# Kernel tuning notes

Hardware: AMD Instinct MI355X
Metric: run time of the kernel (lower is better)

The kernel has to match this reference:

```python
import jax, jax.numpy as jnp
import numpy as np

N_NODES = 170000
N_EDGES = 1200000
IN_C, HID_C, OUT_C = 128, 128, 40
BN_EPS = 1e-5


def setup_inputs() -> dict:
    key = jax.random.key(0)
    ks = jax.random.split(key, 12)
    def glorot(k, fan_in, fan_out):
        lim = (6.0 / (fan_in + fan_out)) ** 0.5
        return jax.random.uniform(k, (fan_in, fan_out), jnp.float32, -lim, lim)
    x = jax.random.normal(ks[0], (N_NODES, IN_C), jnp.float32)
    edge_index = jax.random.randint(ks[1], (2, N_EDGES), 0, N_NODES, jnp.int64)
    return {
        "x": x,
        "edge_index": edge_index,
        "W0": glorot(ks[2], IN_C, HID_C), "b0": jnp.zeros((HID_C,), jnp.float32),
        "g0": jnp.ones((HID_C,), jnp.float32), "be0": jnp.zeros((HID_C,), jnp.float32),
        "W1": glorot(ks[3], HID_C, HID_C), "b1": jnp.zeros((HID_C,), jnp.float32),
        "g1": jnp.ones((HID_C,), jnp.float32), "be1": jnp.zeros((HID_C,), jnp.float32),
        "W2": glorot(ks[4], HID_C, OUT_C), "b2": jnp.zeros((OUT_C,), jnp.float32),
    }


def _gcn_norm(edge_index, num_nodes):
    # add self-loops, symmetric normalization (PyG GCNConv default)
    loop = jnp.arange(num_nodes, dtype=edge_index.dtype)
    src = jnp.concatenate([edge_index[0], loop])
    dst = jnp.concatenate([edge_index[1], loop])
    deg = jax.ops.segment_sum(jnp.ones_like(dst, jnp.float32), dst, num_segments=num_nodes)
    dinv = jnp.where(deg > 0, jax.lax.rsqrt(deg), 0.0)
    norm = dinv[src] * dinv[dst]  # [E+N]
    return src, dst, norm


def _conv(h, W, b, src, dst, norm, num_nodes):
    h = h @ W                              # [N, out]
    msg = h[src] * norm[:, None]           # gather + scale, [E+N, out]
    out = jax.ops.segment_sum(msg, dst, num_segments=num_nodes)
    return out + b


def _bn_relu(h, g, be):
    mean = jnp.mean(h, axis=0)
    var = jnp.mean(jnp.square(h - mean), axis=0)  # biased, as torch BN training
    h = (h - mean) * jax.lax.rsqrt(var + BN_EPS) * g + be
    return jax.nn.relu(h)


def reference(x, edge_index, W0, b0, g0, be0, W1, b1, g1, be1, W2, b2):
    N = x.shape[0]
    src, dst, norm = _gcn_norm(edge_index, N)
    h = _bn_relu(_conv(x, W0, b0, src, dst, norm, N), g0, be0)
    h = _bn_relu(_conv(h, W1, b1, src, dst, norm, N), g1, be1)
    return _conv(h, W2, b2, src, dst, norm, N)
```

## Files before the change

### kernel.cpp

```cpp
#include <hip/hip_runtime.h>

#define BN_EPS 1e-5f
#define CAP 3072

using bf16x8 = __attribute__((ext_vector_type(8))) short;
using f32x4  = __attribute__((ext_vector_type(4))) float;

__device__ __forceinline__ unsigned int f2bf(float f) {
    unsigned int u = __float_as_uint(f);
    u += 0x7fffu + ((u >> 16) & 1u);
    return u >> 16;
}
__device__ __forceinline__ float bflo(unsigned int u) { return __uint_as_float(u << 16); }
__device__ __forceinline__ float bfhi(unsigned int u) { return __uint_as_float(u & 0xffff0000u); }

__global__ __launch_bounds__(1024) void k_init(int* __restrict__ bcur,
                                               float* __restrict__ stats, int NB) {
    int t = threadIdx.x;
    if (t < NB) bcur[t] = t * CAP;
    if (t < 512) stats[t] = 0.f;
}

__global__ __launch_bounds__(256) void k_bscatter(const int* __restrict__ ei,
                                                  int* __restrict__ bcur,
                                                  unsigned int* __restrict__ ebuf,
                                                  int E, int NB) {
    __shared__ int h[768];
    __shared__ int wb[768];
    for (int i = threadIdx.x; i < 768; i += 256) h[i] = 0;
    __syncthreads();
    int base = blockIdx.x * 8192;
    int rk[32];
    #pragma unroll
    for (int it = 0; it < 32; ++it) {
        int e = base + it * 256 + threadIdx.x;
        rk[it] = (e < E) ? atomicAdd(&h[ei[E + e] >> 8], 1) : 0;
    }
    __syncthreads();
    for (int i = threadIdx.x; i < NB; i += 256) {
        int c = h[i];
        wb[i] = c ? atomicAdd(&bcur[i], c) : 0;
    }
    __syncthreads();
    #pragma unroll
    for (int it = 0; it < 32; ++it) {
        int e = base + it * 256 + threadIdx.x;
        if (e < E) {
            unsigned s = (unsigned)ei[e], d = (unsigned)ei[E + e];
            int bk = (int)(d >> 8);
            int pos = wb[bk] + rk[it];
            if (pos < (bk + 1) * CAP)
                ebuf[pos] = s | ((d & 255u) << 24);
        }
    }
}

__global__ __launch_bounds__(256) void k_bfinal(const unsigned int* __restrict__ ebuf,
                                                const int* __restrict__ bcur,
                                                int* __restrict__ csr,
                                                int* __restrict__ rs,
                                                int* __restrict__ re,
                                                float* __restrict__ dinv, int N) {
    __shared__ int cnt[256];
    __shared__ int scn[256];
    __shared__ int cur[256];
    const int t = threadIdx.x, b = blockIdx.x;
    const int beg = b * CAP;
    const int cntE = min(bcur[b] - beg, CAP);
    cnt[t] = 0;
    __syncthreads();
    for (int j = t; j < cntE; j += 256)
        atomicAdd(&cnt[ebuf[beg + j] >> 24], 1);
    __syncthreads();
    int v = cnt[t];
    scn[t] = v;
    __syncthreads();
    for (int off = 1; off < 256; off <<= 1) {
        int x = (t >= off) ? scn[t - off] : 0;
        __syncthreads();
        scn[t] += x;
        __syncthreads();
    }
    int excl = scn[t] - v;
    int node = b * 256 + t;
    if (node < N) {
        rs[node]   = beg + excl;
        re[node]   = beg + excl + v;
        dinv[node] = rsqrtf((float)(1 + v));
    }
    cur[t] = beg + excl;
    __syncthreads();
    for (int j = t; j < cntE; j += 256) {
        unsigned e = ebuf[beg + j];
        int pos = atomicAdd(&cur[e >> 24], 1);
        csr[pos] = (int)(e & 0x00FFFFFFu);
    }
}

__global__ __launch_bounds__(256) void k_prepW3(const float* __restrict__ W0,
                                                const float* __restrict__ W1,
                                                const float* __restrict__ W2,
                                                unsigned short* __restrict__ Wf) {
    int t = blockIdx.x * 256 + threadIdx.x;
    int wid = t >> 11;
    int f = t & 2047;
    const float* W = (wid == 0) ? W0 : (wid == 1) ? W1 : W2;
    int C = (wid == 2) ? 40 : 128;
    int lane = f & 63, frag = f >> 6;
    int kt = frag & 3, ct = frag >> 2;
    int r = lane & 15, q = lane >> 4;
    int col = ct * 16 + r;
    int kbase = kt * 32 + q * 8;
    unsigned int v[8];
    #pragma unroll
    for (int j = 0; j < 8; ++j)
        v[j] = (col < C) ? f2bf(W[(size_t)(kbase + j) * C + col]) : 0u;
    uint4 o;
    o.x = v[0] | (v[1] << 16);
    o.y = v[2] | (v[3] << 16);
    o.z = v[4] | (v[5] << 16);
    o.w = v[6] | (v[7] << 16);
    ((uint4*)Wf)[t] = o;
}

__device__ __forceinline__ float bn_apply(float v, int c, const float* stats,
                                          const float* g, const float* be, float invN) {
    float mean = stats[c] * invN;
    float var  = fmaf(-mean, mean, stats[128 + c] * invN);
    float sc   = g[c] * rsqrtf(var + BN_EPS);
    float r    = fmaf(v - mean, sc, be[c]);
    return fmaxf(r, 0.0f);
}

template <int NOCT, int OST>
__global__ __launch_bounds__(256) void k_gemm_mfma(
        const void* __restrict__ X, int xf32, const unsigned short* __restrict__ Wf,
        unsigned short* __restrict__ H, int N,
        const float* __restrict__ stats, const float* __restrict__ g,
        const float* __restrict__ be) {
    __shared__ unsigned short aF[16 * 512];
    __shared__ unsigned short bF[NOCT * 4 * 512];
    const int tid = threadIdx.x;
    const int rowbase = blockIdx.x * 64;
    const float invN = 1.0f / (float)N;

    {
        const uint4* src = (const uint4*)Wf;
        uint4* dst = (uint4*)bF;
        #pragma unroll
        for (int i = 0; i < NOCT; ++i) dst[tid + 256 * i] = src[tid + 256 * i];
    }
    #pragma unroll
    for (int it = 0; it < 4; ++it) {
        int f = tid + 256 * it;
        int lane = f & 63, frag = f >> 6;
        int kt = frag & 3, rt = frag >> 2;
        int r = lane & 15, q = lane >> 4;
        int row = rowbase + rt * 16 + r;
        int kc = kt * 32 + q * 8;
        float vv[8];
        if (row < N) {
            if (xf32) {
                const float4* xp = (const float4*)((const float*)X + (size_t)row * 128 + kc);
                float4 p0 = xp[0], p1 = xp[1];
                vv[0] = p0.x; vv[1] = p0.y; vv[2] = p0.z; vv[3] = p0.w;
                vv[4] = p1.x; vv[5] = p1.y; vv[6] = p1.z; vv[7] = p1.w;
            } else {
                uint4 p = *((const uint4*)((const unsigned short*)X + (size_t)row * 128 + kc));
                vv[0] = bflo(p.x); vv[1] = bfhi(p.x);
                vv[2] = bflo(p.y); vv[3] = bfhi(p.y);
                vv[4] = bflo(p.z); vv[5] = bfhi(p.z);
                vv[6] = bflo(p.w); vv[7] = bfhi(p.w);
            }
            if (stats) {
                #pragma unroll
                for (int j = 0; j < 8; ++j)
                    vv[j] = bn_apply(vv[j], kc + j, stats, g, be, invN);
            }
        } else {
            #pragma unroll
            for (int j = 0; j < 8; ++j) vv[j] = 0.0f;
        }
        uint4 o;
        o.x = f2bf(vv[0]) | (f2bf(vv[1]) << 16);
        o.y = f2bf(vv[2]) | (f2bf(vv[3]) << 16);
        o.z = f2bf(vv[4]) | (f2bf(vv[5]) << 16);
        o.w = f2bf(vv[6]) | (f2bf(vv[7]) << 16);
        ((uint4*)aF)[f] = o;
    }
    __syncthreads();

    const int wave = tid >> 6, lane = tid & 63;
    f32x4 acc[NOCT];
    #pragma unroll
    for (int ct = 0; ct < NOCT; ++ct) acc[ct] = (f32x4){0.f, 0.f, 0.f, 0.f};

    #pragma unroll
    for (int kt = 0; kt < 4; ++kt) {
        bf16x8 a = ((const bf16x8*)aF)[(wave * 4 + kt) * 64 + lane];
        #pragma unroll
        for (int ct = 0; ct < NOCT; ++ct) {
            bf16x8 b = ((const bf16x8*)bF)[(ct * 4 + kt) * 64 + lane];
            acc[ct] = __builtin_amdgcn_mfma_f32_16x16x32_bf16(a, b, acc[ct], 0, 0, 0);
        }
    }

    const int q = lane >> 4, r = lane & 15;
    #pragma unroll
    for (int ct = 0; ct < NOCT; ++ct) {
        #pragma unroll
        for (int i = 0; i < 4; ++i) {
            int row = rowbase + wave * 16 + q * 4 + i;
            if (row < N)
                H[(size_t)row * OST + ct * 16 + r] = (unsigned short)f2bf(acc[ct][i]);
        }
    }
}

__global__ __launch_bounds__(256) void k_agg128(
        const unsigned short* __restrict__ H, const int* __restrict__ rs,
        const int* __restrict__ re, const int* __restrict__ csr,
        const float* __restrict__ dinv, const float* __restrict__ b,
        unsigned short* __restrict__ outb, int N) {
    int lane = threadIdx.x & 15;
    int node = blockIdx.x * 16 + (threadIdx.x >> 4);
    if (node >= N) return;
    float dd  = dinv[node];
    int   beg = rs[node];
    int   end = re[node];
    uint4 hp  = ((const uint4*)(H + (size_t)node * 128))[lane];
    float4 bb0 = ((const float4*)b)[lane * 2];
    float4 bb1 = ((const float4*)b)[lane * 2 + 1];
    float sl = dd * dd;
    float a0 = fmaf(bflo(hp.x), sl, bb0.x), a1 = fmaf(bfhi(hp.x), sl, bb0.y);
    float a2 = fmaf(bflo(hp.y), sl, bb0.z), a3 = fmaf(bfhi(hp.y), sl, bb0.w);
    float a4 = fmaf(bflo(hp.z), sl, bb1.x), a5 = fmaf(bfhi(hp.z), sl, bb1.y);
    float a6 = fmaf(bflo(hp.w), sl, bb1.z), a7 = fmaf(bfhi(hp.w), sl, bb1.w);
    int j = beg;
    for (; j + 2 <= end; j += 2) {
        int s0 = csr[j], s1 = csr[j + 1];
        float n0 = dinv[s0] * dd, n1 = dinv[s1] * dd;
        uint4 v0 = ((const uint4*)(H + (size_t)s0 * 128))[lane];
        uint4 v1 = ((const uint4*)(H + (size_t)s1 * 128))[lane];
        a0 = fmaf(bflo(v0.x), n0, fmaf(bflo(v1.x), n1, a0));
        a1 = fmaf(bfhi(v0.x), n0, fmaf(bfhi(v1.x), n1, a1));
        a2 = fmaf(bflo(v0.y), n0, fmaf(bflo(v1.y), n1, a2));
        a3 = fmaf(bfhi(v0.y), n0, fmaf(bfhi(v1.y), n1, a3));
        a4 = fmaf(bflo(v0.z), n0, fmaf(bflo(v1.z), n1, a4));
        a5 = fmaf(bfhi(v0.z), n0, fmaf(bfhi(v1.z), n1, a5));
        a6 = fmaf(bflo(v0.w), n0, fmaf(bflo(v1.w), n1, a6));
        a7 = fmaf(bfhi(v0.w), n0, fmaf(bfhi(v1.w), n1, a7));
    }
    if (j < end) {
        int s0 = csr[j];
        float n0 = dinv[s0] * dd;
        uint4 v0 = ((const uint4*)(H + (size_t)s0 * 128))[lane];
        a0 = fmaf(bflo(v0.x), n0, a0); a1 = fmaf(bfhi(v0.x), n0, a1);
        a2 = fmaf(bflo(v0.y), n0, a2); a3 = fmaf(bfhi(v0.y), n0, a3);
        a4 = fmaf(bflo(v0.z), n0, a4); a5 = fmaf(bfhi(v0.z), n0, a5);
        a6 = fmaf(bflo(v0.w), n0, a6); a7 = fmaf(bfhi(v0.w), n0, a7);
    }
    uint4 o;
    o.x = f2bf(a0) | (f2bf(a1) << 16);
    o.y = f2bf(a2) | (f2bf(a3) << 16);
    o.z = f2bf(a4) | (f2bf(a5) << 16);
    o.w = f2bf(a6) | (f2bf(a7) << 16);
    ((uint4*)(outb + (size_t)node * 128))[lane] = o;
}

__global__ __launch_bounds__(256) void k_agg40(
        const unsigned short* __restrict__ H, const int* __restrict__ rs,
        const int* __restrict__ re, const int* __restrict__ csr,
        const float* __restrict__ dinv, const float* __restrict__ b,
        float* __restrict__ out, int N) {
    int lane = threadIdx.x & 15;
    int node = blockIdx.x * 16 + (threadIdx.x >> 4);
    if (node >= N || lane >= 10) return;
    float dd  = dinv[node];
    int   beg = rs[node];
    int   end = re[node];
    uint2 hp  = ((const uint2*)(H + (size_t)node * 48))[lane];
    float4 bb = ((const float4*)b)[lane];
    float  sl = dd * dd;
    float4 acc = make_float4(fmaf(bflo(hp.x), sl, bb.x), fmaf(bfhi(hp.x), sl, bb.y),
                             fmaf(bflo(hp.y), sl, bb.z), fmaf(bfhi(hp.y), sl, bb.w));
    int j = beg;
    for (; j + 2 <= end; j += 2) {
        int s0 = csr[j], s1 = csr[j + 1];
        float n0 = dinv[s0] * dd, n1 = dinv[s1] * dd;
        uint2 v0 = ((const uint2*)(H + (size_t)s0 * 48))[lane];
        uint2 v1 = ((const uint2*)(H + (size_t)s1 * 48))[lane];
        acc.x = fmaf(bflo(v0.x), n0, fmaf(bflo(v1.x), n1, acc.x));
        acc.y = fmaf(bfhi(v0.x), n0, fmaf(bfhi(v1.x), n1, acc.y));
        acc.z = fmaf(bflo(v0.y), n0, fmaf(bflo(v1.y), n1, acc.z));
        acc.w = fmaf(bfhi(v0.y), n0, fmaf(bfhi(v1.y), n1, acc.w));
    }
    if (j < end) {
        int s0 = csr[j];
        float n0 = dinv[s0] * dd;
        uint2 v0 = ((const uint2*)(H + (size_t)s0 * 48))[lane];
        acc.x = fmaf(bflo(v0.x), n0, acc.x);
        acc.y = fmaf(bfhi(v0.x), n0, acc.y);
        acc.z = fmaf(bflo(v0.y), n0, acc.z);
        acc.w = fmaf(bfhi(v0.y), n0, acc.w);
    }
    ((float4*)(out + (size_t)node * 40))[lane] = acc;
}

__global__ __launch_bounds__(256) void k_bnstats(
        const unsigned short* __restrict__ Bb, float* __restrict__ stats, int N) {
    __shared__ float red[2][16][128];
    const int t = threadIdx.x;
    const int lane16 = t & 15, grp = t >> 4;
    const int cbase = lane16 * 8;
    float s[8], q[8];
    #pragma unroll
    for (int k = 0; k < 8; ++k) { s[k] = 0.f; q[k] = 0.f; }

    const int step = gridDim.x * 16;
    for (int r = blockIdx.x * 16 + grp; r < N; r += 2 * step) {
        uint4 p0 = *((const uint4*)(Bb + (size_t)r * 128 + cbase));
        int r1 = r + step;
        if (r1 < N) {
            uint4 p1 = *((const uint4*)(Bb + (size_t)r1 * 128 + cbase));
            float v[8] = {bflo(p1.x), bfhi(p1.x), bflo(p1.y), bfhi(p1.y),
                          bflo(p1.z), bfhi(p1.z), bflo(p1.w), bfhi(p1.w)};
            #pragma unroll
            for (int k = 0; k < 8; ++k) { s[k] += v[k]; q[k] = fmaf(v[k], v[k], q[k]); }
        }
        float u[8] = {bflo(p0.x), bfhi(p0.x), bflo(p0.y), bfhi(p0.y),
                      bflo(p0.z), bfhi(p0.z), bflo(p0.w), bfhi(p0.w)};
        #pragma unroll
        for (int k = 0; k < 8; ++k) { s[k] += u[k]; q[k] = fmaf(u[k], u[k], q[k]); }
    }
    #pragma unroll
    for (int k = 0; k < 8; ++k) {
        red[0][grp][cbase + k] = s[k];
        red[1][grp][cbase + k] = q[k];
    }
    __syncthreads();
    if (t < 128) {
        float acc = 0.f;
        #pragma unroll
        for (int g = 0; g < 16; ++g) acc += red[0][g][t];
        unsafeAtomicAdd(&stats[t], acc);
    } else {
        int c = t - 128;
        float acc = 0.f;
        #pragma unroll
        for (int g = 0; g < 16; ++g) acc += red[1][g][c];
        unsafeAtomicAdd(&stats[128 + c], acc);
    }
}

extern "C" void kernel_launch(void* const* d_in, const int* in_sizes, int n_in,
                              void* d_out, int out_size, void* d_ws, size_t ws_size,
                              hipStream_t stream) {
    const float* x   = (const float*)d_in[0];
    const int*   ei  = (const int*)d_in[1];
    const float* W0  = (const float*)d_in[2];
    const float* b0  = (const float*)d_in[3];
    const float* g0  = (const float*)d_in[4];
    const float* be0 = (const float*)d_in[5];
    const float* W1  = (const float*)d_in[6];
    const float* b1  = (const float*)d_in[7];
    const float* g1  = (const float*)d_in[8];
    const float* be1 = (const float*)d_in[9];
    const float* W2  = (const float*)d_in[10];
    const float* b2  = (const float*)d_in[11];
    float* out = (float*)d_out;

    const int N  = in_sizes[0] / 128;
    const int E  = in_sizes[1] / 2;
    const int NB = (N + 255) >> 8;
    const int EB = (E + 8191) / 8192;

    float* ws   = (float*)d_ws;
    size_t Npad = ((size_t)N + 511) & ~(size_t)511;
    size_t BCAP = (size_t)NB * CAP;
    float* dinv = ws;
    int*   rs   = (int*)(ws + Npad);
    int*   re   = rs + Npad;
    int*   csr  = re + Npad;
    unsigned int* ebuf = (unsigned int*)(csr + BCAP);
    int*   bcur = (int*)(ebuf + BCAP);
    float* stats0 = (float*)(bcur + 1024);
    float* stats1 = stats0 + 256;
    unsigned short* Wf = (unsigned short*)(stats1 + 256);
    unsigned short* Hb = Wf + 3 * 16384;
    unsigned short* Bb = Hb + Npad * 128;

    k_init    <<<1, 1024, 0, stream>>>(bcur, stats0, NB);
    k_bscatter<<<EB, 256, 0, stream>>>(ei, bcur, ebuf, E, NB);
    k_bfinal  <<<NB, 256, 0, stream>>>(ebuf, bcur, csr, rs, re, dinv, N);
    k_prepW3  <<<24, 256, 0, stream>>>(W0, W1, W2, Wf);

    int gemm_grid = (N + 63) / 64;
    int agg_grid  = (N + 15) / 16;

    k_gemm_mfma<8, 128><<<gemm_grid, 256, 0, stream>>>(x, 1, Wf, Hb, N,
                                                       nullptr, nullptr, nullptr);
    k_agg128<<<agg_grid, 256, 0, stream>>>(Hb, rs, re, csr, dinv, b0, Bb, N);
    k_bnstats<<<512, 256, 0, stream>>>(Bb, stats0, N);

    k_gemm_mfma<8, 128><<<gemm_grid, 256, 0, stream>>>(Bb, 0, Wf + 16384, Hb, N,
                                                       stats0, g0, be0);
    k_agg128<<<agg_grid, 256, 0, stream>>>(Hb, rs, re, csr, dinv, b1, Bb, N);
    k_bnstats<<<512, 256, 0, stream>>>(Bb, stats1, N);

    k_gemm_mfma<3, 48><<<gemm_grid, 256, 0, stream>>>(Bb, 0, Wf + 2 * 16384, Hb, N,
                                                      stats1, g1, be1);
    k_agg40<<<agg_grid, 256, 0, stream>>>(Hb, rs, re, csr, dinv, b2, out, N);
}
```

Before: 473.4 us.

## Assign one wavefront per node in aggregation kernels with 4-way edge unrolling

Changes the aggregation kernels from 16 lanes per node (each loading 16 bytes) to a full 64-lane wavefront per node (each loading 4 bytes), with node index made wave-uniform via readfirstlane. The edge loop is unrolled by 4 to keep more gathers in flight per wave. The aim is uniform control flow per wave and more memory-level parallelism, at the cost of fewer nodes per block and narrower per-lane loads. In the 40-channel kernel, 44 of 64 lanes are idle.

```diff
diff --git a/kernel.cpp b/kernel.cpp
--- a/kernel.cpp
+++ b/kernel.cpp
@@ -222,50 +222,50 @@
         const int* __restrict__ re, const int* __restrict__ csr,
         const float* __restrict__ dinv, const float* __restrict__ b,
         unsigned short* __restrict__ outb, int N) {
-    int lane = threadIdx.x & 15;
-    int node = blockIdx.x * 16 + (threadIdx.x >> 4);
+    const int lane = threadIdx.x & 63;
+    const int wid  = __builtin_amdgcn_readfirstlane(threadIdx.x >> 6);
+    const int node = blockIdx.x * 4 + wid;
     if (node >= N) return;
-    float dd  = dinv[node];
-    int   beg = rs[node];
-    int   end = re[node];
-    uint4 hp  = ((const uint4*)(H + (size_t)node * 128))[lane];
-    float4 bb0 = ((const float4*)b)[lane * 2];
-    float4 bb1 = ((const float4*)b)[lane * 2 + 1];
-    float sl = dd * dd;
-    float a0 = fmaf(bflo(hp.x), sl, bb0.x), a1 = fmaf(bfhi(hp.x), sl, bb0.y);
-    float a2 = fmaf(bflo(hp.y), sl, bb0.z), a3 = fmaf(bfhi(hp.y), sl, bb0.w);
-    float a4 = fmaf(bflo(hp.z), sl, bb1.x), a5 = fmaf(bfhi(hp.z), sl, bb1.y);
-    float a6 = fmaf(bflo(hp.w), sl, bb1.z), a7 = fmaf(bfhi(hp.w), sl, bb1.w);
+    const unsigned int* __restrict__ Hd = (const unsigned int*)H;
+    const float dd  = dinv[node];
+    const int   beg = rs[node];
+    const int   end = re[node];
+    unsigned int hp = Hd[(size_t)node * 64 + lane];
+    float2 bb = ((const float2*)b)[lane];
+    float  sl = dd * dd;
+    float a0 = fmaf(bflo(hp), sl, bb.x);
+    float a1 = fmaf(bfhi(hp), sl, bb.y);
     int j = beg;
-    for (; j + 2 <= end; j += 2) {
+    for (; j + 4 <= end; j += 4) {
+        int s0 = csr[j], s1 = csr[j + 1], s2 = csr[j + 2], s3 = csr[j + 3];
+        float n0 = dinv[s0] * dd, n1 = dinv[s1] * dd;
+        float n2 = dinv[s2] * dd, n3 = dinv[s3] * dd;
+        unsigned int v0 = Hd[(size_t)s0 * 64 + lane];
+        unsigned int v1 = Hd[(size_t)s1 * 64 + lane];
+        unsigned int v2 = Hd[(size_t)s2 * 64 + lane];
+        unsigned int v3 = Hd[(size_t)s3 * 64 + lane];
+        a0 = fmaf(bflo(v0), n0, a0); a1 = fmaf(bfhi(v0), n0, a1);
+        a0 = fmaf(bflo(v1), n1, a0); a1 = fmaf(bfhi(v1), n1, a1);
+        a0 = fmaf(bflo(v2), n2, a0); a1 = fmaf(bfhi(v2), n2, a1);
+        a0 = fmaf(bflo(v3), n3, a0); a1 = fmaf(bfhi(v3), n3, a1);
+    }
+    if (j + 2 <= end) {
         int s0 = csr[j], s1 = csr[j + 1];
         float n0 = dinv[s0] * dd, n1 = dinv[s1] * dd;
-        uint4 v0 = ((const uint4*)(H + (size_t)s0 * 128))[lane];
-        uint4 v1 = ((const uint4*)(H + (size_t)s1 * 128))[lane];
-        a0 = fmaf(bflo(v0.x), n0, fmaf(bflo(v1.x), n1, a0));
-        a1 = fmaf(bfhi(v0.x), n0, fmaf(bfhi(v1.x), n1, a1));
-        a2 = fmaf(bflo(v0.y), n0, fmaf(bflo(v1.y), n1, a2));
-        a3 = fmaf(bfhi(v0.y), n0, fmaf(bfhi(v1.y), n1, a3));
-        a4 = fmaf(bflo(v0.z), n0, fmaf(bflo(v1.z), n1, a4));
-        a5 = fmaf(bfhi(v0.z), n0, fmaf(bfhi(v1.z), n1, a5));
-        a6 = fmaf(bflo(v0.w), n0, fmaf(bflo(v1.w), n1, a6));
-        a7 = fmaf(bfhi(v0.w), n0, fmaf(bfhi(v1.w), n1, a7));
+        unsigned int v0 = Hd[(size_t)s0 * 64 + lane];
+        unsigned int v1 = Hd[(size_t)s1 * 64 + lane];
+        a0 = fmaf(bflo(v0), n0, a0); a1 = fmaf(bfhi(v0), n0, a1);
+        a0 = fmaf(bflo(v1), n1, a0); a1 = fmaf(bfhi(v1), n1, a1);
+        j += 2;
     }
     if (j < end) {
         int s0 = csr[j];
         float n0 = dinv[s0] * dd;
-        uint4 v0 = ((const uint4*)(H + (size_t)s0 * 128))[lane];
-        a0 = fmaf(bflo(v0.x), n0, a0); a1 = fmaf(bfhi(v0.x), n0, a1);
-        a2 = fmaf(bflo(v0.y), n0, a2); a3 = fmaf(bfhi(v0.y), n0, a3);
-        a4 = fmaf(bflo(v0.z), n0, a4); a5 = fmaf(bfhi(v0.z), n0, a5);
-        a6 = fmaf(bflo(v0.w), n0, a6); a7 = fmaf(bfhi(v0.w), n0, a7);
-    }
-    uint4 o;
-    o.x = f2bf(a0) | (f2bf(a1) << 16);
-    o.y = f2bf(a2) | (f2bf(a3) << 16);
-    o.z = f2bf(a4) | (f2bf(a5) << 16);
-    o.w = f2bf(a6) | (f2bf(a7) << 16);
-    ((uint4*)(outb + (size_t)node * 128))[lane] = o;
+        unsigned int v0 = Hd[(size_t)s0 * 64 + lane];
+        a0 = fmaf(bflo(v0), n0, a0); a1 = fmaf(bfhi(v0), n0, a1);
+    }
+    unsigned int o = f2bf(a0) | (f2bf(a1) << 16);
+    ((unsigned int*)outb)[(size_t)node * 64 + lane] = o;
 }
 
 __global__ __launch_bounds__(256) void k_agg40(
@@ -273,38 +273,52 @@
         const int* __restrict__ re, const int* __restrict__ csr,
         const float* __restrict__ dinv, const float* __restrict__ b,
         float* __restrict__ out, int N) {
-    int lane = threadIdx.x & 15;
-    int node = blockIdx.x * 16 + (threadIdx.x >> 4);
-    if (node >= N || lane >= 10) return;
-    float dd  = dinv[node];
-    int   beg = rs[node];
-    int   end = re[node];
-    uint2 hp  = ((const uint2*)(H + (size_t)node * 48))[lane];
-    float4 bb = ((const float4*)b)[lane];
+    const int lane = threadIdx.x & 63;
+    const int wid  = __builtin_amdgcn_readfirstlane(threadIdx.x >> 6);
+    const int node = blockIdx.x * 4 + wid;
+    if (node >= N) return;
+    const bool act = lane < 20;
+    const int  ll  = act ? lane : 0;
+    const unsigned int* __restrict__ Hd = (const unsigned int*)H;
+    const float dd  = dinv[node];
+    const int   beg = rs[node];
+    const int   end = re[node];
+    unsigned int hp = Hd[(size_t)node * 24 + ll];
+    float2 bb = ((const float2*)b)[ll];
     float  sl = dd * dd;
-    float4 acc = make_float4(fmaf(bflo(hp.x), sl, bb.x), fmaf(bfhi(hp.x), sl, bb.y),
-                             fmaf(bflo(hp.y), sl, bb.z), fmaf(bfhi(hp.y), sl, bb.w));
+    float a0 = fmaf(bflo(hp), sl, bb.x);
+    float a1 = fmaf(bfhi(hp), sl, bb.y);
     int j = beg;
-    for (; j + 2 <= end; j += 2) {
+    for (; j + 4 <= end; j += 4) {
+        int s0 = csr[j], s1 = csr[j + 1], s2 = csr[j + 2], s3 = csr[j + 3];
+        float n0 = dinv[s0] * dd, n1 = dinv[s1] * dd;
+        float n2 = dinv[s2] * dd, n3 = dinv[s3] * dd;
+        unsigned int v0 = Hd[(size_t)s0 * 24 + ll];
+        unsigned int v1 = Hd[(size_t)s1 * 24 + ll];
+        unsigned int v2 = Hd[(size_t)s2 * 24 + ll];
+        unsigned int v3 = Hd[(size_t)s3 * 24 + ll];
+        a0 = fmaf(bflo(v0), n0, a0); a1 = fmaf(bfhi(v0), n0, a1);
+        a0 = fmaf(bflo(v1), n1, a0); a1 = fmaf(bfhi(v1), n1, a1);
+        a0 = fmaf(bflo(v2), n2, a0); a1 = fmaf(bfhi(v2), n2, a1);
+        a0 = fmaf(bflo(v3), n3, a0); a1 = fmaf(bfhi(v3), n3, a1);
+    }
+    if (j + 2 <= end) {
         int s0 = csr[j], s1 = csr[j + 1];
         float n0 = dinv[s0] * dd, n1 = dinv[s1] * dd;
-        uint2 v0 = ((const uint2*)(H + (size_t)s0 * 48))[lane];
-        uint2 v1 = ((const uint2*)(H + (size_t)s1 * 48))[lane];
-        acc.x = fmaf(bflo(v0.x), n0, fmaf(bflo(v1.x), n1, acc.x));
-        acc.y = fmaf(bfhi(v0.x), n0, fmaf(bfhi(v1.x), n1, acc.y));
-        acc.z = fmaf(bflo(v0.y), n0, fmaf(bflo(v1.y), n1, acc.z));
-        acc.w = fmaf(bfhi(v0.y), n0, fmaf(bfhi(v1.y), n1, acc.w));
+        unsigned int v0 = Hd[(size_t)s0 * 24 + ll];
+        unsigned int v1 = Hd[(size_t)s1 * 24 + ll];
+        a0 = fmaf(bflo(v0), n0, a0); a1 = fmaf(bfhi(v0), n0, a1);
+        a0 = fmaf(bflo(v1), n1, a0); a1 = fmaf(bfhi(v1), n1, a1);
+        j += 2;
     }
     if (j < end) {
         int s0 = csr[j];
         float n0 = dinv[s0] * dd;
-        uint2 v0 = ((const uint2*)(H + (size_t)s0 * 48))[lane];
-        acc.x = fmaf(bflo(v0.x), n0, acc.x);
-        acc.y = fmaf(bfhi(v0.x), n0, acc.y);
-        acc.z = fmaf(bflo(v0.y), n0, acc.z);
-        acc.w = fmaf(bfhi(v0.y), n0, acc.w);
-    }
-    ((float4*)(out + (size_t)node * 40))[lane] = acc;
+        unsigned int v0 = Hd[(size_t)s0 * 24 + ll];
+        a0 = fmaf(bflo(v0), n0, a0); a1 = fmaf(bfhi(v0), n0, a1);
+    }
+    if (act)
+        ((float2*)(out + (size_t)node * 40))[lane] = make_float2(a0, a1);
 }
 
 __global__ __launch_bounds__(256) void k_bnstats(
@@ -396,7 +410,7 @@
     k_prepW3  <<<24, 256, 0, stream>>>(W0, W1, W2, Wf);
 
     int gemm_grid = (N + 63) / 64;
-    int agg_grid  = (N + 15) / 16;
+    int agg_grid  = (N + 3) / 4;
 
     k_gemm_mfma<8, 128><<<gemm_grid, 256, 0, stream>>>(x, 1, Wf, Hb, N,
                                                        nullptr, nullptr, nullptr);
```

Result: slower. 497.4 us (+5.1%).

## Fuse BatchNorm statistics into aggregation kernel and fold init into weight prep

Applied to the files above, without the earlier changes.

The 128-wide aggregation kernel becomes grid-stride with a fixed grid of 2048 blocks. It accumulates per-channel sums and sums of squares in registers, reduces them through shared memory, and adds them to the stats buffers with atomics, so the separate bnstats pass that re-read the aggregated output is removed. The init kernel is merged into the weight-prep kernel to save a launch. Stats now come from the fp32 accumulators rather than the bf16-rounded stored values, and a fixed grid size may change load balance and occupancy for the irregular gather.

```diff
diff --git a/kernel.cpp b/kernel.cpp
--- a/kernel.cpp
+++ b/kernel.cpp
@@ -13,13 +13,6 @@
 }
 __device__ __forceinline__ float bflo(unsigned int u) { return __uint_as_float(u << 16); }
 __device__ __forceinline__ float bfhi(unsigned int u) { return __uint_as_float(u & 0xffff0000u); }
-
-__global__ __launch_bounds__(1024) void k_init(int* __restrict__ bcur,
-                                               float* __restrict__ stats, int NB) {
-    int t = threadIdx.x;
-    if (t < NB) bcur[t] = t * CAP;
-    if (t < 512) stats[t] = 0.f;
-}
 
 __global__ __launch_bounds__(256) void k_bscatter(const int* __restrict__ ei,
                                                   int* __restrict__ bcur,
@@ -100,8 +93,12 @@
 __global__ __launch_bounds__(256) void k_prepW3(const float* __restrict__ W0,
                                                 const float* __restrict__ W1,
                                                 const float* __restrict__ W2,
-                                                unsigned short* __restrict__ Wf) {
+                                                unsigned short* __restrict__ Wf,
+                                                int* __restrict__ bcur,
+                                                float* __restrict__ stats, int NB) {
     int t = blockIdx.x * 256 + threadIdx.x;
+    if (t < NB) bcur[t] = t * CAP;
+    if (t < 512) stats[t] = 0.f;
     int wid = t >> 11;
     int f = t & 2047;
     const float* W = (wid == 0) ? W0 : (wid == 1) ? W1 : W2;
@@ -221,51 +218,85 @@
         const unsigned short* __restrict__ H, const int* __restrict__ rs,
         const int* __restrict__ re, const int* __restrict__ csr,
         const float* __restrict__ dinv, const float* __restrict__ b,
-        unsigned short* __restrict__ outb, int N) {
-    int lane = threadIdx.x & 15;
-    int node = blockIdx.x * 16 + (threadIdx.x >> 4);
-    if (node >= N) return;
-    float dd  = dinv[node];
-    int   beg = rs[node];
-    int   end = re[node];
-    uint4 hp  = ((const uint4*)(H + (size_t)node * 128))[lane];
+        unsigned short* __restrict__ outb, float* __restrict__ stats, int N) {
+    __shared__ float red[2][16][128];
+    const int t = threadIdx.x;
+    const int lane = t & 15, grp = t >> 4;
     float4 bb0 = ((const float4*)b)[lane * 2];
     float4 bb1 = ((const float4*)b)[lane * 2 + 1];
-    float sl = dd * dd;
-    float a0 = fmaf(bflo(hp.x), sl, bb0.x), a1 = fmaf(bfhi(hp.x), sl, bb0.y);
-    float a2 = fmaf(bflo(hp.y), sl, bb0.z), a3 = fmaf(bfhi(hp.y), sl, bb0.w);
-    float a4 = fmaf(bflo(hp.z), sl, bb1.x), a5 = fmaf(bfhi(hp.z), sl, bb1.y);
-    float a6 = fmaf(bflo(hp.w), sl, bb1.z), a7 = fmaf(bfhi(hp.w), sl, bb1.w);
-    int j = beg;
-    for (; j + 2 <= end; j += 2) {
-        int s0 = csr[j], s1 = csr[j + 1];
-        float n0 = dinv[s0] * dd, n1 = dinv[s1] * dd;
-        uint4 v0 = ((const uint4*)(H + (size_t)s0 * 128))[lane];
-        uint4 v1 = ((const uint4*)(H + (size_t)s1 * 128))[lane];
-        a0 = fmaf(bflo(v0.x), n0, fmaf(bflo(v1.x), n1, a0));
-        a1 = fmaf(bfhi(v0.x), n0, fmaf(bfhi(v1.x), n1, a1));
-        a2 = fmaf(bflo(v0.y), n0, fmaf(bflo(v1.y), n1, a2));
-        a3 = fmaf(bfhi(v0.y), n0, fmaf(bfhi(v1.y), n1, a3));
-        a4 = fmaf(bflo(v0.z), n0, fmaf(bflo(v1.z), n1, a4));
-        a5 = fmaf(bfhi(v0.z), n0, fmaf(bfhi(v1.z), n1, a5));
-        a6 = fmaf(bflo(v0.w), n0, fmaf(bflo(v1.w), n1, a6));
-        a7 = fmaf(bfhi(v0.w), n0, fmaf(bfhi(v1.w), n1, a7));
-    }
-    if (j < end) {
-        int s0 = csr[j];
-        float n0 = dinv[s0] * dd;
-        uint4 v0 = ((const uint4*)(H + (size_t)s0 * 128))[lane];
-        a0 = fmaf(bflo(v0.x), n0, a0); a1 = fmaf(bfhi(v0.x), n0, a1);
-        a2 = fmaf(bflo(v0.y), n0, a2); a3 = fmaf(bfhi(v0.y), n0, a3);
-        a4 = fmaf(bflo(v0.z), n0, a4); a5 = fmaf(bfhi(v0.z), n0, a5);
-        a6 = fmaf(bflo(v0.w), n0, a6); a7 = fmaf(bfhi(v0.w), n0, a7);
-    }
-    uint4 o;
-    o.x = f2bf(a0) | (f2bf(a1) << 16);
-    o.y = f2bf(a2) | (f2bf(a3) << 16);
-    o.z = f2bf(a4) | (f2bf(a5) << 16);
-    o.w = f2bf(a6) | (f2bf(a7) << 16);
-    ((uint4*)(outb + (size_t)node * 128))[lane] = o;
+    float s[8], q[8];
+    #pragma unroll
+    for (int k = 0; k < 8; ++k) { s[k] = 0.f; q[k] = 0.f; }
+
+    const int step = gridDim.x * 16;
+    for (int node = blockIdx.x * 16 + grp; node < N; node += step) {
+        float dd  = dinv[node];
+        int   beg = rs[node];
+        int   end = re[node];
+        uint4 hp  = ((const uint4*)(H + (size_t)node * 128))[lane];
+        float sl = dd * dd;
+        float a0 = fmaf(bflo(hp.x), sl, bb0.x), a1 = fmaf(bfhi(hp.x), sl, bb0.y);
+        float a2 = fmaf(bflo(hp.y), sl, bb0.z), a3 = fmaf(bfhi(hp.y), sl, bb0.w);
+        float a4 = fmaf(bflo(hp.z), sl, bb1.x), a5 = fmaf(bfhi(hp.z), sl, bb1.y);
+        float a6 = fmaf(bflo(hp.w), sl, bb1.z), a7 = fmaf(bfhi(hp.w), sl, bb1.w);
+        int j = beg;
+        for (; j + 2 <= end; j += 2) {
+            int s0 = csr[j], s1 = csr[j + 1];
+            float n0 = dinv[s0] * dd, n1 = dinv[s1] * dd;
+            uint4 v0 = ((const uint4*)(H + (size_t)s0 * 128))[lane];
+            uint4 v1 = ((const uint4*)(H + (size_t)s1 * 128))[lane];
+            a0 = fmaf(bflo(v0.x), n0, fmaf(bflo(v1.x), n1, a0));
+            a1 = fmaf(bfhi(v0.x), n0, fmaf(bfhi(v1.x), n1, a1));
+            a2 = fmaf(bflo(v0.y), n0, fmaf(bflo(v1.y), n1, a2));
+            a3 = fmaf(bfhi(v0.y), n0, fmaf(bfhi(v1.y), n1, a3));
+            a4 = fmaf(bflo(v0.z), n0, fmaf(bflo(v1.z), n1, a4));
+            a5 = fmaf(bfhi(v0.z), n0, fmaf(bfhi(v1.z), n1, a5));
+            a6 = fmaf(bflo(v0.w), n0, fmaf(bflo(v1.w), n1, a6));
+            a7 = fmaf(bfhi(v0.w), n0, fmaf(bfhi(v1.w), n1, a7));
+        }
+        if (j < end) {
+            int s0 = csr[j];
+            float n0 = dinv[s0] * dd;
+            uint4 v0 = ((const uint4*)(H + (size_t)s0 * 128))[lane];
+            a0 = fmaf(bflo(v0.x), n0, a0); a1 = fmaf(bfhi(v0.x), n0, a1);
+            a2 = fmaf(bflo(v0.y), n0, a2); a3 = fmaf(bfhi(v0.y), n0, a3);
+            a4 = fmaf(bflo(v0.z), n0, a4); a5 = fmaf(bfhi(v0.z), n0, a5);
+            a6 = fmaf(bflo(v0.w), n0, a6); a7 = fmaf(bfhi(v0.w), n0, a7);
+        }
+        uint4 o;
+        o.x = f2bf(a0) | (f2bf(a1) << 16);
+        o.y = f2bf(a2) | (f2bf(a3) << 16);
+        o.z = f2bf(a4) | (f2bf(a5) << 16);
+        o.w = f2bf(a6) | (f2bf(a7) << 16);
+        ((uint4*)(outb + (size_t)node * 128))[lane] = o;
+        s[0] += a0; q[0] = fmaf(a0, a0, q[0]);
+        s[1] += a1; q[1] = fmaf(a1, a1, q[1]);
+        s[2] += a2; q[2] = fmaf(a2, a2, q[2]);
+        s[3] += a3; q[3] = fmaf(a3, a3, q[3]);
+        s[4] += a4; q[4] = fmaf(a4, a4, q[4]);
+        s[5] += a5; q[5] = fmaf(a5, a5, q[5]);
+        s[6] += a6; q[6] = fmaf(a6, a6, q[6]);
+        s[7] += a7; q[7] = fmaf(a7, a7, q[7]);
+    }
+    #pragma unroll
+    for (int k = 0; k < 8; ++k) {
+        red[0][grp][lane * 8 + k] = s[k];
+        red[1][grp][lane * 8 + k] = q[k];
+    }
+    __syncthreads();
+    if (t < 128) {
+        int c = (t + (blockIdx.x << 2)) & 127;
+        float acc = 0.f;
+        #pragma unroll
+        for (int g = 0; g < 16; ++g) acc += red[0][g][c];
+        unsafeAtomicAdd(&stats[c], acc);
+    } else {
+        int c = ((t - 128) + (blockIdx.x << 2)) & 127;
+        float acc = 0.f;
+        #pragma unroll
+        for (int g = 0; g < 16; ++g) acc += red[1][g][c];
+        unsafeAtomicAdd(&stats[128 + c], acc);
+    }
 }
 
 __global__ __launch_bounds__(256) void k_agg40(
@@ -307,52 +338,6 @@
     ((float4*)(out + (size_t)node * 40))[lane] = acc;
 }
 
-__global__ __launch_bounds__(256) void k_bnstats(
-        const unsigned short* __restrict__ Bb, float* __restrict__ stats, int N) {
-    __shared__ float red[2][16][128];
-    const int t = threadIdx.x;
-    const int lane16 = t & 15, grp = t >> 4;
-    const int cbase = lane16 * 8;
-    float s[8], q[8];
-    #pragma unroll
-    for (int k = 0; k < 8; ++k) { s[k] = 0.f; q[k] = 0.f; }
-
-    const int step = gridDim.x * 16;
-    for (int r = blockIdx.x * 16 + grp; r < N; r += 2 * step) {
-        uint4 p0 = *((const uint4*)(Bb + (size_t)r * 128 + cbase));
-        int r1 = r + step;
-        if (r1 < N) {
-            uint4 p1 = *((const uint4*)(Bb + (size_t)r1 * 128 + cbase));
-            float v[8] = {bflo(p1.x), bfhi(p1.x), bflo(p1.y), bfhi(p1.y),
-                          bflo(p1.z), bfhi(p1.z), bflo(p1.w), bfhi(p1.w)};
-            #pragma unroll
-            for (int k = 0; k < 8; ++k) { s[k] += v[k]; q[k] = fmaf(v[k], v[k], q[k]); }
-        }
-        float u[8] = {bflo(p0.x), bfhi(p0.x), bflo(p0.y), bfhi(p0.y),
-                      bflo(p0.z), bfhi(p0.z), bflo(p0.w), bfhi(p0.w)};
-        #pragma unroll
-        for (int k = 0; k < 8; ++k) { s[k] += u[k]; q[k] = fmaf(u[k], u[k], q[k]); }
-    }
-    #pragma unroll
-    for (int k = 0; k < 8; ++k) {
-        red[0][grp][cbase + k] = s[k];
-        red[1][grp][cbase + k] = q[k];
-    }
-    __syncthreads();
-    if (t < 128) {
-        float acc = 0.f;
-        #pragma unroll
-        for (int g = 0; g < 16; ++g) acc += red[0][g][t];
-        unsafeAtomicAdd(&stats[t], acc);
-    } else {
-        int c = t - 128;
-        float acc = 0.f;
-        #pragma unroll
-        for (int g = 0; g < 16; ++g) acc += red[1][g][c];
-        unsafeAtomicAdd(&stats[128 + c], acc);
-    }
-}
-
 extern "C" void kernel_launch(void* const* d_in, const int* in_sizes, int n_in,
                               void* d_out, int out_size, void* d_ws, size_t ws_size,
                               hipStream_t stream) {
@@ -390,25 +375,23 @@
     unsigned short* Hb = Wf + 3 * 16384;
     unsigned short* Bb = Hb + Npad * 128;
 
-    k_init    <<<1, 1024, 0, stream>>>(bcur, stats0, NB);
+    k_prepW3  <<<24, 256, 0, stream>>>(W0, W1, W2, Wf, bcur, stats0, NB);
     k_bscatter<<<EB, 256, 0, stream>>>(ei, bcur, ebuf, E, NB);
     k_bfinal  <<<NB, 256, 0, stream>>>(ebuf, bcur, csr, rs, re, dinv, N);
-    k_prepW3  <<<24, 256, 0, stream>>>(W0, W1, W2, Wf);
 
     int gemm_grid = (N + 63) / 64;
-    int agg_grid  = (N + 15) / 16;
+    int agg_grid  = 2048;
+    int agg40_grid = (N + 15) / 16;
 
     k_gemm_mfma<8, 128><<<gemm_grid, 256, 0, stream>>>(x, 1, Wf, Hb, N,
                                                        nullptr, nullptr, nullptr);
-    k_agg128<<<agg_grid, 256, 0, stream>>>(Hb, rs, re, csr, dinv, b0, Bb, N);
-    k_bnstats<<<512, 256, 0, stream>>>(Bb, stats0, N);
+    k_agg128<<<agg_grid, 256, 0, stream>>>(Hb, rs, re, csr, dinv, b0, Bb, stats0, N);
 
     k_gemm_mfma<8, 128><<<gemm_grid, 256, 0, stream>>>(Bb, 0, Wf + 16384, Hb, N,
                                                        stats0, g0, be0);
-    k_agg128<<<agg_grid, 256, 0, stream>>>(Hb, rs, re, csr, dinv, b1, Bb, N);
-    k_bnstats<<<512, 256, 0, stream>>>(Bb, stats1, N);
+    k_agg128<<<agg_grid, 256, 0, stream>>>(Hb, rs, re, csr, dinv, b1, Bb, stats1, N);
 
     k_gemm_mfma<3, 48><<<gemm_grid, 256, 0, stream>>>(Bb, 0, Wf + 2 * 16384, Hb, N,
                                                       stats1, g1, be1);
-    k_agg40<<<agg_grid, 256, 0, stream>>>(Hb, rs, re, csr, dinv, b2, out, N);
-}
+    k_agg40<<<agg40_grid, 256, 0, stream>>>(Hb, rs, re, csr, dinv, b2, out, N);
+}
```

New measurement: 550.8 us. 1.16x slower.
